# Optimization experiments

Measured on AMD Instinct MI355X. Metric: run time of the kernel, lower is better.

## Reference

```python
import jax, jax.numpy as jnp
from jax import lax
import numpy as np

TAO, M, C_IN, D_MODEL = 3, 5, 7, 512
KERNELS = D_MODEL // C_IN            # 73
EXTRA = D_MODEL - C_IN * KERNELS     # 1


def setup_inputs() -> dict:
    key = jax.random.key(0)
    k1, k2, k3, k4, k5 = jax.random.split(key, 5)
    B, S = 32, 4096
    x = jax.random.normal(k1, (B, S, C_IN), dtype=jnp.float32)
    fan_in = (M + 1) * 3
    scale = jnp.float32(np.sqrt(2.0 / fan_in))  # kaiming-ish
    group_w = jax.random.normal(k2, (C_IN * KERNELS, M + 1, 3), dtype=jnp.float32) * scale
    group_b = jax.random.normal(k3, (C_IN * KERNELS,), dtype=jnp.float32) * 0.01
    left_w = jax.random.normal(k4, (EXTRA, M + 1, 3), dtype=jnp.float32) * scale
    left_b = jax.random.normal(k5, (EXTRA,), dtype=jnp.float32) * 0.01
    return {"x": x, "group_w": group_w, "group_b": group_b,
            "left_w": left_w, "left_b": left_b}


def _circular_conv1d(x_ncl, w_oik, groups):
    # kernel_size=3, padding=1, padding_mode='circular' -> wrap-pad then VALID conv
    xp = jnp.pad(x_ncl, ((0, 0), (0, 0), (1, 1)), mode="wrap")
    return lax.conv_general_dilated(
        xp, w_oik, window_strides=(1,), padding="VALID",
        dimension_numbers=("NCH", "OIH", "NCH"),
        feature_group_count=groups)


def reference(x, group_w, group_b, left_w, left_b):
    B, S, C = x.shape
    warm = M * TAO
    # vectorized delay-embedding gather: faithful vec at time t is
    # [ts[t - i*tao, c] for c in channels for i in 0..m]  (channel-major)
    times = jnp.arange(warm, S)                              # [T']
    lags = times[:, None] - TAO * jnp.arange(M + 1)[None, :]  # [T', m+1]
    g = x[:, lags, :]                                        # [B, T', m+1, C]
    g = jnp.transpose(g, (0, 1, 3, 2)).reshape(B, S - warm, C * (M + 1))
    # pad warmup region with zeros at the front of the time axis
    g = jnp.pad(g, ((0, 0), (warm, 0), (0, 0)))              # [B, S, C*(m+1)]
    e = jnp.transpose(g, (0, 2, 1))                          # [B, C*(m+1), S]
    conv = _circular_conv1d(e, group_w, groups=C_IN) + group_b[None, :, None]
    # leftout conv on the last channel's delay block
    last = e.reshape(B, C_IN, M + 1, S)[:, -1]               # [B, m+1, S]
    extra = _circular_conv1d(last, left_w, groups=1) + left_b[None, :, None]
    out = jnp.concatenate([conv, extra], axis=1)             # [B, d_model, S]
    return jnp.transpose(out, (0, 2, 1))                     # [B, S, d_model]
```

## Files before the change

### kernel.cpp

```cpp
#include <hip/hip_runtime.h>

#define S_LEN 4096
#define B_SZ 32
#define C_IN 7
#define D_MODEL 512
#define TL 64
#define NL 16

__global__ __launch_bounds__(512)
void fir_main(const float* __restrict__ x,
              const float* __restrict__ gw,
              const float* __restrict__ gb,
              const float* __restrict__ lw,
              const float* __restrict__ lb,
              float* __restrict__ out)
{
    const int o  = threadIdx.x;
    const int n  = blockIdx.x;
    const int l0 = blockIdx.y * TL;

    const int c = (o < 511) ? (o / 73) : 6;
    const float* wsrc = (o < 511) ? (gw + o * 18) : lw;
    const float bias  = (o < 511) ? gb[o] : lb[0];

    float wf[18];
#pragma unroll
    for (int j = 0; j < 6; ++j)
#pragma unroll
        for (int k = 0; k < 3; ++k)
            wf[15 + k - 3 * j] = wsrc[j * 3 + k];

    const float* xc = x + (size_t)n * S_LEN * C_IN + c;
    float* op = out + ((size_t)n * S_LEN + l0) * D_MODEL + o;

#pragma unroll
    for (int mi = 0; mi < TL / NL; ++mi) {
        const int lb_ = l0 + mi * NL;
        float xv[NL + 17];
#pragma unroll
        for (int d = 0; d < NL + 17; ++d) {
            int t = lb_ - 16 + d;
            t = t < 0 ? 0 : t;
            t = t > (S_LEN - 1) ? (S_LEN - 1) : t;
            xv[d] = xc[(size_t)t * C_IN];
        }
#pragma unroll
        for (int u = 0; u < NL; ++u) {
            float acc = bias;
#pragma unroll
            for (int d = 0; d < 18; ++d)
                acc = fmaf(wf[d], xv[u + d], acc);
            op[(size_t)(mi * NL + u) * D_MODEL] = acc;
        }
    }
}

__global__ __launch_bounds__(512)
void fir_fixup(const float* __restrict__ x,
               const float* __restrict__ gw,
               const float* __restrict__ gb,
               const float* __restrict__ lw,
               const float* __restrict__ lb,
               float* __restrict__ out)
{
    const int o  = threadIdx.x;
    const int n  = blockIdx.x;
    const int li = blockIdx.y;
    const int l  = (li < 16) ? li : (S_LEN - 1);

    const int c = (o < 511) ? (o / 73) : 6;
    const float* wsrc = (o < 511) ? (gw + o * 18) : lw;
    float acc = (o < 511) ? gb[o] : lb[0];

    const float* xc = x + (size_t)n * S_LEN * C_IN + c;
#pragma unroll
    for (int j = 0; j < 6; ++j) {
#pragma unroll
        for (int k = 0; k < 3; ++k) {
            int t = l - 1 + k;
            if (t < 0) t += S_LEN;
            if (t >= S_LEN) t -= S_LEN;
            if (t >= 15)
                acc = fmaf(wsrc[j * 3 + k], xc[(size_t)(t - 3 * j) * C_IN], acc);
        }
    }
    out[((size_t)n * S_LEN + l) * D_MODEL + o] = acc;
}

extern "C" void kernel_launch(void* const* d_in, const int* in_sizes, int n_in,
                              void* d_out, int out_size, void* d_ws, size_t ws_size,
                              hipStream_t stream)
{
    const float* x  = (const float*)d_in[0];
    const float* gw = (const float*)d_in[1];
    const float* gb = (const float*)d_in[2];
    const float* lw = (const float*)d_in[3];
    const float* lb = (const float*)d_in[4];
    float* out = (float*)d_out;

    dim3 grid_main(B_SZ, S_LEN / TL);
    fir_main<<<grid_main, 512, 0, stream>>>(x, gw, gb, lw, lb, out);

    dim3 grid_fix(B_SZ, 17);
    fir_fixup<<<grid_fix, 512, 0, stream>>>(x, gw, gb, lw, lb, out);
}
```

Measured before the change: 298.9 us.

## Stage weights and input window in LDS with vectorized float4 reads

The main kernel now cooperatively loads all filter weights, biases and the block's clamped input time window into shared memory. Each thread then reads its weights and input samples from LDS, using float4 loads in chunks of 8 outputs instead of 16. This replaces many strided scalar global loads of x per thread. In exchange it adds about 40KB of shared memory per block and a block barrier, which may limit occupancy, and the weight staging is repeated in every block.

```diff
diff --git a/kernel.cpp b/kernel.cpp
--- a/kernel.cpp
+++ b/kernel.cpp
@@ -5,7 +5,8 @@
 #define C_IN 7
 #define D_MODEL 512
 #define TL 64
-#define NL 16
+#define CH 8
+#define NCH (TL / CH)
 
 __global__ __launch_bounds__(512)
 void fir_main(const float* __restrict__ x,
@@ -15,42 +16,55 @@
               const float* __restrict__ lb,
               float* __restrict__ out)
 {
-    const int o  = threadIdx.x;
-    const int n  = blockIdx.x;
-    const int l0 = blockIdx.y * TL;
+    __shared__ float ws[512 * 18];
+    __shared__ float wb[512];
+    __shared__ float xs[7][88];
 
+    const int tid = threadIdx.x;
+    const int n   = blockIdx.x;
+    const int l0  = blockIdx.y * TL;
+
+    for (int i = tid; i < 512 * 18; i += 512)
+        ws[i] = (i < 511 * 18) ? gw[i] : lw[i - 511 * 18];
+    wb[tid] = (tid < 511) ? gb[tid] : lb[0];
+
+    for (int i = tid; i < 81 * 7; i += 512) {
+        int t = i / 7, c = i - t * 7;
+        int tg = l0 - 16 + t;
+        tg = tg < 0 ? 0 : (tg > S_LEN - 1 ? S_LEN - 1 : tg);
+        xs[c][t] = x[((size_t)n * S_LEN + tg) * C_IN + c];
+    }
+    __syncthreads();
+
+    const int o = tid;
     const int c = (o < 511) ? (o / 73) : 6;
-    const float* wsrc = (o < 511) ? (gw + o * 18) : lw;
-    const float bias  = (o < 511) ? gb[o] : lb[0];
-
     float wf[18];
 #pragma unroll
     for (int j = 0; j < 6; ++j)
 #pragma unroll
         for (int k = 0; k < 3; ++k)
-            wf[15 + k - 3 * j] = wsrc[j * 3 + k];
+            wf[15 + k - 3 * j] = ws[o * 18 + j * 3 + k];
+    const float bias = wb[o];
 
-    const float* xc = x + (size_t)n * S_LEN * C_IN + c;
     float* op = out + ((size_t)n * S_LEN + l0) * D_MODEL + o;
 
 #pragma unroll
-    for (int mi = 0; mi < TL / NL; ++mi) {
-        const int lb_ = l0 + mi * NL;
-        float xv[NL + 17];
+    for (int ci = 0; ci < NCH; ++ci) {
+        float xv[28];
+        const float* xb = &xs[c][ci * CH];
 #pragma unroll
-        for (int d = 0; d < NL + 17; ++d) {
-            int t = lb_ - 16 + d;
-            t = t < 0 ? 0 : t;
-            t = t > (S_LEN - 1) ? (S_LEN - 1) : t;
-            xv[d] = xc[(size_t)t * C_IN];
+        for (int q = 0; q < 7; ++q) {
+            float4 v = *(const float4*)(xb + q * 4);
+            xv[q * 4 + 0] = v.x; xv[q * 4 + 1] = v.y;
+            xv[q * 4 + 2] = v.z; xv[q * 4 + 3] = v.w;
         }
 #pragma unroll
-        for (int u = 0; u < NL; ++u) {
+        for (int u = 0; u < CH; ++u) {
             float acc = bias;
 #pragma unroll
             for (int d = 0; d < 18; ++d)
                 acc = fmaf(wf[d], xv[u + d], acc);
-            op[(size_t)(mi * NL + u) * D_MODEL] = acc;
+            op[(size_t)(ci * CH + u) * D_MODEL] = acc;
         }
     }
 }
```

New measurement: 284.5 us. -4.8%, faster.
